# Optimization experiments

Measured on AMD Instinct MI355X. Metric: run time of the kernel, lower is better.

Reference implementation:

```python
import jax, jax.numpy as jnp
import numpy as np

IN_FEATURES = 128
OUT_FEATURES = 32
N_NODES = 2048
ALPHA = 0.2  # LeakyReLU negative slope
NEG_INF = -9e15


def setup_inputs() -> dict:
    key = jax.random.key(0)
    k1, k2, k3, k4 = jax.random.split(key, 4)
    h = jax.random.normal(k1, (N_NODES, IN_FEATURES), dtype=jnp.float32)
    adj = jax.random.randint(k2, (N_NODES, N_NODES), 0, 2, dtype=jnp.int32)
    # xavier_uniform-ish scaling for params
    W = jax.random.normal(k3, (2 * IN_FEATURES, OUT_FEATURES), dtype=jnp.float32) * 0.1
    a = jax.random.normal(k4, (OUT_FEATURES,), dtype=jnp.float32) * 0.2
    return {"h": h, "adj": adj, "W": W, "a": a}


def reference(h, adj, W, a):
    in_f = h.shape[1]
    Wh1 = h @ W[:in_f, :]   # [N, F]
    Wh2 = h @ W[in_f:, :]   # [N, F]
    # GATv2 score: e[i,k] = sum_f a[f] * leaky_relu(Wh1[i,f] + Wh2[k,f])
    e = jax.nn.leaky_relu(Wh1[:, None, :] + Wh2[None, :, :], negative_slope=ALPHA)  # [N, N, F]
    e = jnp.einsum('ikf,f->ik', e, a)  # [N, N]
    att = jnp.where(adj > 0, e, NEG_INF)
    att = jax.nn.softmax(att, axis=1)
    h_prime = att @ Wh1  # note: original aggregates Wh1, faithful to source
    return jax.nn.elu(h_prime)  # concat=True -> ELU
```

## Files before the change

### kernel.cpp

```cpp
#include <hip/hip_runtime.h>
#include <math.h>

#define N_NODES 2048
#define IN_F 128
#define OUT_F 32
#define NEG_INF -9e15f

__device__ __forceinline__ int swz(int k) { return k ^ (((k >> 7) & 7) << 2); }

__global__ __launch_bounds__(256) void precompute_wh(
    const float* __restrict__ h, const float* __restrict__ W,
    const float* __restrict__ a,
    float* __restrict__ Wh1, float* __restrict__ Wh2,
    float* __restrict__ Q, float* __restrict__ C)
{
    __shared__ float h_s[8][IN_F];
    const int t = threadIdx.x;
    const int i0 = blockIdx.x * 8;

    ((float4*)&h_s[0][0])[t] = ((const float4*)(h + (size_t)i0 * IN_F))[t];
    __syncthreads();

    const int f = t & 31;
    const int r = t >> 5;
    float acc1 = 0.f, acc2 = 0.f;
    #pragma unroll 8
    for (int c = 0; c < IN_F; ++c) {
        const float hv = h_s[r][c];
        acc1 = fmaf(hv, W[c * OUT_F + f], acc1);
        acc2 = fmaf(hv, W[(IN_F + c) * OUT_F + f], acc2);
    }
    Wh1[(i0 + r) * OUT_F + f] = acc1;
    Wh2[(i0 + r) * OUT_F + f] = acc2;

    float q = 0.6f * a[f] * acc2;
    #pragma unroll
    for (int off = 16; off > 0; off >>= 1) q += __shfl_xor(q, off, 64);
    if (f == 0) Q[i0 + r] = q;

    if (blockIdx.x == 0 && t < OUT_F) C[t] = 0.4f * a[t];
}

__global__ __launch_bounds__(256, 4) void gat_row(
    const float* __restrict__ Wh1, const float* __restrict__ Wh2,
    const float* __restrict__ Q, const float* __restrict__ C,
    const int* __restrict__ adj, float* __restrict__ out)
{
    __shared__ float p_s[2 * N_NODES];
    __shared__ float w1s[2][OUT_F];
    __shared__ float part[16][2][OUT_F];
    __shared__ float redA[4], redB[4], redC[4], redD[4];

    const int t = threadIdx.x;
    const int i0 = blockIdx.x * 2;

    if (t < 2 * OUT_F) w1s[t >> 5][t & 31] = Wh1[i0 * OUT_F + t];
    __syncthreads();

    const float4* w1f0 = (const float4*)&w1s[0][0];
    const float4* w1f1 = (const float4*)&w1s[1][0];

    float s00[4], s01[4], s10[4], s11[4];
    float m0 = NEG_INF, m1 = NEG_INF;

    #pragma unroll
    for (int kc = 0; kc < 4; ++kc) {
        const int k = 2 * t + 512 * kc;
        const float4* wr = (const float4*)(Wh2 + (size_t)k * OUT_F);
        float a00 = 0.f, a01 = 0.f, a10 = 0.f, a11 = 0.f;
        #pragma unroll
        for (int j = 0; j < 8; ++j) {
            const float4 w1a = w1f0[j];
            const float4 w1b = w1f1[j];
            const float4 qa = wr[j];
            const float4 qb = wr[8 + j];
            #pragma unroll
            for (int e = 0; e < 4; ++e) {
                const float cf  = C[4 * j + e];
                const float w2a = (e==0)?qa.x:(e==1)?qa.y:(e==2)?qa.z:qa.w;
                const float w2b = (e==0)?qb.x:(e==1)?qb.y:(e==2)?qb.z:qb.w;
                const float w10 = (e==0)?w1a.x:(e==1)?w1a.y:(e==2)?w1a.z:w1a.w;
                const float w11 = (e==0)?w1b.x:(e==1)?w1b.y:(e==2)?w1b.z:w1b.w;
                a00 = fmaf(cf, fabsf(w10 + w2a), a00);
                a01 = fmaf(cf, fabsf(w10 + w2b), a01);
                a10 = fmaf(cf, fabsf(w11 + w2a), a10);
                a11 = fmaf(cf, fabsf(w11 + w2b), a11);
            }
        }
        const int2 ad0   = *(const int2*)(adj + (size_t)(i0 + 0) * N_NODES + k);
        const int2 ad1   = *(const int2*)(adj + (size_t)(i0 + 1) * N_NODES + k);
        const float2 qk  = *(const float2*)(Q + k);
        const float v00 = (ad0.x > 0) ? a00 + qk.x : NEG_INF;
        const float v01 = (ad0.y > 0) ? a01 + qk.y : NEG_INF;
        const float v10 = (ad1.x > 0) ? a10 + qk.x : NEG_INF;
        const float v11 = (ad1.y > 0) ? a11 + qk.y : NEG_INF;
        s00[kc] = v00; s01[kc] = v01; s10[kc] = v10; s11[kc] = v11;
        m0 = fmaxf(m0, fmaxf(v00, v01));
        m1 = fmaxf(m1, fmaxf(v10, v11));
    }

    #pragma unroll
    for (int off = 32; off > 0; off >>= 1) {
        m0 = fmaxf(m0, __shfl_xor(m0, off, 64));
        m1 = fmaxf(m1, __shfl_xor(m1, off, 64));
    }
    const int lane = t & 63, wid = t >> 6;
    if (lane == 0) { redA[wid] = m0; redB[wid] = m1; }
    __syncthreads();
    const float M0 = fmaxf(fmaxf(redA[0], redA[1]), fmaxf(redA[2], redA[3]));
    const float M1 = fmaxf(fmaxf(redB[0], redB[1]), fmaxf(redB[2], redB[3]));

    float l0 = 0.f, l1 = 0.f;
    #pragma unroll
    for (int kc = 0; kc < 4; ++kc) {
        const int k = 2 * t + 512 * kc;
        const float p00 = __expf(s00[kc] - M0);
        const float p01 = __expf(s01[kc] - M0);
        const float p10 = __expf(s10[kc] - M1);
        const float p11 = __expf(s11[kc] - M1);
        *(float2*)&p_s[swz(k)]           = make_float2(p00, p01);
        *(float2*)&p_s[N_NODES + swz(k)] = make_float2(p10, p11);
        l0 += p00 + p01;
        l1 += p10 + p11;
    }
    #pragma unroll
    for (int off = 32; off > 0; off >>= 1) {
        l0 += __shfl_xor(l0, off, 64);
        l1 += __shfl_xor(l1, off, 64);
    }
    if (lane == 0) { redC[wid] = l0; redD[wid] = l1; }
    __syncthreads();
    const float L0 = redC[0] + redC[1] + redC[2] + redC[3];
    const float L1 = redD[0] + redD[1] + redD[2] + redD[3];

    const int f2 = t & 15;
    const int c  = t >> 4;
    float acc00 = 0.f, acc01 = 0.f, acc10 = 0.f, acc11 = 0.f;
    const int kb = c * 128;
    #pragma unroll 4
    for (int it = 0; it < 32; ++it) {
        const int k = kb + 4 * it;
        const float4 p0 = *(const float4*)&p_s[swz(k)];
        const float4 p1 = *(const float4*)&p_s[N_NODES + swz(k)];
        const float* wrow = Wh1 + (size_t)k * OUT_F + f2;
        const float wa0 = wrow[0],  wb0 = wrow[16];
        const float wa1 = wrow[32], wb1 = wrow[48];
        const float wa2 = wrow[64], wb2 = wrow[80];
        const float wa3 = wrow[96], wb3 = wrow[112];
        acc00 = fmaf(p0.x, wa0, acc00); acc01 = fmaf(p0.x, wb0, acc01);
        acc10 = fmaf(p1.x, wa0, acc10); acc11 = fmaf(p1.x, wb0, acc11);
        acc00 = fmaf(p0.y, wa1, acc00); acc01 = fmaf(p0.y, wb1, acc01);
        acc10 = fmaf(p1.y, wa1, acc10); acc11 = fmaf(p1.y, wb1, acc11);
        acc00 = fmaf(p0.z, wa2, acc00); acc01 = fmaf(p0.z, wb2, acc01);
        acc10 = fmaf(p1.z, wa2, acc10); acc11 = fmaf(p1.z, wb2, acc11);
        acc00 = fmaf(p0.w, wa3, acc00); acc01 = fmaf(p0.w, wb3, acc01);
        acc10 = fmaf(p1.w, wa3, acc10); acc11 = fmaf(p1.w, wb3, acc11);
    }
    part[c][0][f2]      = acc00;
    part[c][0][f2 + 16] = acc01;
    part[c][1][f2]      = acc10;
    part[c][1][f2 + 16] = acc11;
    __syncthreads();

    if (t < 2 * OUT_F) {
        const int ii = t >> 5, ff = t & 31;
        float s = 0.f;
        #pragma unroll
        for (int c2 = 0; c2 < 16; ++c2) s += part[c2][ii][ff];
        const float val = s / (ii == 0 ? L0 : L1);
        out[(i0 + ii) * OUT_F + ff] = (val > 0.f) ? val : (__expf(val) - 1.f);
    }
}

extern "C" void kernel_launch(void* const* d_in, const int* in_sizes, int n_in,
                              void* d_out, int out_size, void* d_ws, size_t ws_size,
                              hipStream_t stream) {
    const float* h   = (const float*)d_in[0];
    const int*   adj = (const int*)d_in[1];
    const float* W   = (const float*)d_in[2];
    const float* a   = (const float*)d_in[3];
    float* out = (float*)d_out;

    float* Wh1 = (float*)d_ws;
    float* Wh2 = Wh1 + N_NODES * OUT_F;
    float* Q   = Wh2 + N_NODES * OUT_F;
    float* C   = Q + N_NODES;

    precompute_wh<<<N_NODES / 8, 256, 0, stream>>>(h, W, a, Wh1, Wh2, Q, C);
    gat_row<<<N_NODES / 2, 256, 0, stream>>>(Wh1, Wh2, Q, C, adj, out);
}
```

Measured before the change: 125.2 us.

## Transpose Wh2 and process four rows per block for register reuse

The precompute kernel now writes Wh2 transposed (feature-major) through a shared-memory staging tile, so the score loop can load float4 runs of neighbour values per feature with coalesced access. The row kernel handles four query rows per block instead of two. Each thread computes 4x8 scores, which reuses each loaded Wh2 value across four rows and halves how often Wh2 and Wh1 are re-read during aggregation. The trade-off is higher register pressure: launch bounds drop to 2 blocks per SM, with fewer blocks in flight and fewer blocks overall.

```diff
diff --git a/kernel.cpp b/kernel.cpp
--- a/kernel.cpp
+++ b/kernel.cpp
@@ -11,10 +11,11 @@
 __global__ __launch_bounds__(256) void precompute_wh(
     const float* __restrict__ h, const float* __restrict__ W,
     const float* __restrict__ a,
-    float* __restrict__ Wh1, float* __restrict__ Wh2,
+    float* __restrict__ Wh1, float* __restrict__ Wh2T,
     float* __restrict__ Q, float* __restrict__ C)
 {
     __shared__ float h_s[8][IN_F];
+    __shared__ float tr[8][OUT_F];
     const int t = threadIdx.x;
     const int i0 = blockIdx.x * 8;
 
@@ -31,143 +32,175 @@
         acc2 = fmaf(hv, W[(IN_F + c) * OUT_F + f], acc2);
     }
     Wh1[(i0 + r) * OUT_F + f] = acc1;
-    Wh2[(i0 + r) * OUT_F + f] = acc2;
+    tr[r][f] = acc2;
 
     float q = 0.6f * a[f] * acc2;
     #pragma unroll
     for (int off = 16; off > 0; off >>= 1) q += __shfl_xor(q, off, 64);
     if (f == 0) Q[i0 + r] = q;
-
     if (blockIdx.x == 0 && t < OUT_F) C[t] = 0.4f * a[t];
+
+    __syncthreads();
+    const int f2 = t >> 3, r2 = t & 7;
+    Wh2T[f2 * N_NODES + i0 + r2] = tr[r2][f2];
 }
 
-__global__ __launch_bounds__(256, 4) void gat_row(
-    const float* __restrict__ Wh1, const float* __restrict__ Wh2,
+__global__ __launch_bounds__(256, 2) void gat_row(
+    const float* __restrict__ Wh1, const float* __restrict__ Wh2T,
     const float* __restrict__ Q, const float* __restrict__ C,
     const int* __restrict__ adj, float* __restrict__ out)
 {
-    __shared__ float p_s[2 * N_NODES];
-    __shared__ float w1s[2][OUT_F];
-    __shared__ float part[16][2][OUT_F];
-    __shared__ float redA[4], redB[4], redC[4], redD[4];
+    __shared__ float p_s[4][N_NODES];
+    __shared__ float w1s[4][OUT_F];
+    __shared__ float part[16][4][OUT_F];
+    __shared__ float redM[4][4], redL[4][4];
 
     const int t = threadIdx.x;
-    const int i0 = blockIdx.x * 2;
-
-    if (t < 2 * OUT_F) w1s[t >> 5][t & 31] = Wh1[i0 * OUT_F + t];
-    __syncthreads();
-
-    const float4* w1f0 = (const float4*)&w1s[0][0];
-    const float4* w1f1 = (const float4*)&w1s[1][0];
-
-    float s00[4], s01[4], s10[4], s11[4];
-    float m0 = NEG_INF, m1 = NEG_INF;
-
-    #pragma unroll
-    for (int kc = 0; kc < 4; ++kc) {
-        const int k = 2 * t + 512 * kc;
-        const float4* wr = (const float4*)(Wh2 + (size_t)k * OUT_F);
-        float a00 = 0.f, a01 = 0.f, a10 = 0.f, a11 = 0.f;
-        #pragma unroll
-        for (int j = 0; j < 8; ++j) {
-            const float4 w1a = w1f0[j];
-            const float4 w1b = w1f1[j];
-            const float4 qa = wr[j];
-            const float4 qb = wr[8 + j];
+    const int i0 = blockIdx.x * 4;
+
+    if (t < 4 * OUT_F) w1s[t >> 5][t & 31] = Wh1[i0 * OUT_F + t];
+    __syncthreads();
+
+    const int kA = 4 * t;
+    const int kB = N_NODES / 2 + 4 * t;
+
+    int4 adA[4], adB[4];
+    #pragma unroll
+    for (int i = 0; i < 4; ++i) {
+        adA[i] = *(const int4*)(adj + (size_t)(i0 + i) * N_NODES + kA);
+        adB[i] = *(const int4*)(adj + (size_t)(i0 + i) * N_NODES + kB);
+    }
+    const float4 QA = *(const float4*)(Q + kA);
+    const float4 QB = *(const float4*)(Q + kB);
+
+    float acc[4][8];
+    #pragma unroll
+    for (int i = 0; i < 4; ++i)
+        #pragma unroll
+        for (int s = 0; s < 8; ++s) acc[i][s] = 0.f;
+
+    #pragma unroll 2
+    for (int j = 0; j < 8; ++j) {
+        float4 w1v[4];
+        #pragma unroll
+        for (int i = 0; i < 4; ++i) w1v[i] = *(const float4*)&w1s[i][4 * j];
+        #pragma unroll
+        for (int e = 0; e < 4; ++e) {
+            const int f = 4 * j + e;
+            const float cf = C[f];
+            const float4 wA = *(const float4*)(Wh2T + (size_t)f * N_NODES + kA);
+            const float4 wB = *(const float4*)(Wh2T + (size_t)f * N_NODES + kB);
             #pragma unroll
-            for (int e = 0; e < 4; ++e) {
-                const float cf  = C[4 * j + e];
-                const float w2a = (e==0)?qa.x:(e==1)?qa.y:(e==2)?qa.z:qa.w;
-                const float w2b = (e==0)?qb.x:(e==1)?qb.y:(e==2)?qb.z:qb.w;
-                const float w10 = (e==0)?w1a.x:(e==1)?w1a.y:(e==2)?w1a.z:w1a.w;
-                const float w11 = (e==0)?w1b.x:(e==1)?w1b.y:(e==2)?w1b.z:w1b.w;
-                a00 = fmaf(cf, fabsf(w10 + w2a), a00);
-                a01 = fmaf(cf, fabsf(w10 + w2b), a01);
-                a10 = fmaf(cf, fabsf(w11 + w2a), a10);
-                a11 = fmaf(cf, fabsf(w11 + w2b), a11);
+            for (int i = 0; i < 4; ++i) {
+                const float w1 = (e==0)?w1v[i].x:(e==1)?w1v[i].y:(e==2)?w1v[i].z:w1v[i].w;
+                acc[i][0] = fmaf(cf, fabsf(w1 + wA.x), acc[i][0]);
+                acc[i][1] = fmaf(cf, fabsf(w1 + wA.y), acc[i][1]);
+                acc[i][2] = fmaf(cf, fabsf(w1 + wA.z), acc[i][2]);
+                acc[i][3] = fmaf(cf, fabsf(w1 + wA.w), acc[i][3]);
+                acc[i][4] = fmaf(cf, fabsf(w1 + wB.x), acc[i][4]);
+                acc[i][5] = fmaf(cf, fabsf(w1 + wB.y), acc[i][5]);
+                acc[i][6] = fmaf(cf, fabsf(w1 + wB.z), acc[i][6]);
+                acc[i][7] = fmaf(cf, fabsf(w1 + wB.w), acc[i][7]);
             }
         }
-        const int2 ad0   = *(const int2*)(adj + (size_t)(i0 + 0) * N_NODES + k);
-        const int2 ad1   = *(const int2*)(adj + (size_t)(i0 + 1) * N_NODES + k);
-        const float2 qk  = *(const float2*)(Q + k);
-        const float v00 = (ad0.x > 0) ? a00 + qk.x : NEG_INF;
-        const float v01 = (ad0.y > 0) ? a01 + qk.y : NEG_INF;
-        const float v10 = (ad1.x > 0) ? a10 + qk.x : NEG_INF;
-        const float v11 = (ad1.y > 0) ? a11 + qk.y : NEG_INF;
-        s00[kc] = v00; s01[kc] = v01; s10[kc] = v10; s11[kc] = v11;
-        m0 = fmaxf(m0, fmaxf(v00, v01));
-        m1 = fmaxf(m1, fmaxf(v10, v11));
-    }
-
-    #pragma unroll
-    for (int off = 32; off > 0; off >>= 1) {
-        m0 = fmaxf(m0, __shfl_xor(m0, off, 64));
-        m1 = fmaxf(m1, __shfl_xor(m1, off, 64));
+    }
+
+    float m[4];
+    #pragma unroll
+    for (int i = 0; i < 4; ++i) {
+        acc[i][0] = (adA[i].x > 0) ? acc[i][0] + QA.x : NEG_INF;
+        acc[i][1] = (adA[i].y > 0) ? acc[i][1] + QA.y : NEG_INF;
+        acc[i][2] = (adA[i].z > 0) ? acc[i][2] + QA.z : NEG_INF;
+        acc[i][3] = (adA[i].w > 0) ? acc[i][3] + QA.w : NEG_INF;
+        acc[i][4] = (adB[i].x > 0) ? acc[i][4] + QB.x : NEG_INF;
+        acc[i][5] = (adB[i].y > 0) ? acc[i][5] + QB.y : NEG_INF;
+        acc[i][6] = (adB[i].z > 0) ? acc[i][6] + QB.z : NEG_INF;
+        acc[i][7] = (adB[i].w > 0) ? acc[i][7] + QB.w : NEG_INF;
+        float mm = fmaxf(fmaxf(fmaxf(acc[i][0], acc[i][1]), fmaxf(acc[i][2], acc[i][3])),
+                         fmaxf(fmaxf(acc[i][4], acc[i][5]), fmaxf(acc[i][6], acc[i][7])));
+        #pragma unroll
+        for (int off = 32; off > 0; off >>= 1) mm = fmaxf(mm, __shfl_xor(mm, off, 64));
+        m[i] = mm;
     }
     const int lane = t & 63, wid = t >> 6;
-    if (lane == 0) { redA[wid] = m0; redB[wid] = m1; }
-    __syncthreads();
-    const float M0 = fmaxf(fmaxf(redA[0], redA[1]), fmaxf(redA[2], redA[3]));
-    const float M1 = fmaxf(fmaxf(redB[0], redB[1]), fmaxf(redB[2], redB[3]));
-
-    float l0 = 0.f, l1 = 0.f;
-    #pragma unroll
-    for (int kc = 0; kc < 4; ++kc) {
-        const int k = 2 * t + 512 * kc;
-        const float p00 = __expf(s00[kc] - M0);
-        const float p01 = __expf(s01[kc] - M0);
-        const float p10 = __expf(s10[kc] - M1);
-        const float p11 = __expf(s11[kc] - M1);
-        *(float2*)&p_s[swz(k)]           = make_float2(p00, p01);
-        *(float2*)&p_s[N_NODES + swz(k)] = make_float2(p10, p11);
-        l0 += p00 + p01;
-        l1 += p10 + p11;
-    }
-    #pragma unroll
-    for (int off = 32; off > 0; off >>= 1) {
-        l0 += __shfl_xor(l0, off, 64);
-        l1 += __shfl_xor(l1, off, 64);
-    }
-    if (lane == 0) { redC[wid] = l0; redD[wid] = l1; }
-    __syncthreads();
-    const float L0 = redC[0] + redC[1] + redC[2] + redC[3];
-    const float L1 = redD[0] + redD[1] + redD[2] + redD[3];
+    if (lane == 0) {
+        redM[0][wid] = m[0]; redM[1][wid] = m[1];
+        redM[2][wid] = m[2]; redM[3][wid] = m[3];
+    }
+    __syncthreads();
+
+    float L[4];
+    #pragma unroll
+    for (int i = 0; i < 4; ++i) {
+        const float M = fmaxf(fmaxf(redM[i][0], redM[i][1]), fmaxf(redM[i][2], redM[i][3]));
+        const float p0 = __expf(acc[i][0] - M);
+        const float p1 = __expf(acc[i][1] - M);
+        const float p2 = __expf(acc[i][2] - M);
+        const float p3 = __expf(acc[i][3] - M);
+        const float p4 = __expf(acc[i][4] - M);
+        const float p5 = __expf(acc[i][5] - M);
+        const float p6 = __expf(acc[i][6] - M);
+        const float p7 = __expf(acc[i][7] - M);
+        *(float4*)&p_s[i][swz(kA)] = make_float4(p0, p1, p2, p3);
+        *(float4*)&p_s[i][swz(kB)] = make_float4(p4, p5, p6, p7);
+        float ll = (p0 + p1) + (p2 + p3) + ((p4 + p5) + (p6 + p7));
+        #pragma unroll
+        for (int off = 32; off > 0; off >>= 1) ll += __shfl_xor(ll, off, 64);
+        L[i] = ll;
+    }
+    if (lane == 0) {
+        redL[0][wid] = L[0]; redL[1][wid] = L[1];
+        redL[2][wid] = L[2]; redL[3][wid] = L[3];
+    }
+    __syncthreads();
 
     const int f2 = t & 15;
     const int c  = t >> 4;
-    float acc00 = 0.f, acc01 = 0.f, acc10 = 0.f, acc11 = 0.f;
+    float a00=0.f, a01=0.f, a10=0.f, a11=0.f, a20=0.f, a21=0.f, a30=0.f, a31=0.f;
     const int kb = c * 128;
     #pragma unroll 4
     for (int it = 0; it < 32; ++it) {
         const int k = kb + 4 * it;
-        const float4 p0 = *(const float4*)&p_s[swz(k)];
-        const float4 p1 = *(const float4*)&p_s[N_NODES + swz(k)];
+        const int ks = swz(k);
+        const float4 p0 = *(const float4*)&p_s[0][ks];
+        const float4 p1 = *(const float4*)&p_s[1][ks];
+        const float4 p2 = *(const float4*)&p_s[2][ks];
+        const float4 p3 = *(const float4*)&p_s[3][ks];
         const float* wrow = Wh1 + (size_t)k * OUT_F + f2;
         const float wa0 = wrow[0],  wb0 = wrow[16];
         const float wa1 = wrow[32], wb1 = wrow[48];
         const float wa2 = wrow[64], wb2 = wrow[80];
         const float wa3 = wrow[96], wb3 = wrow[112];
-        acc00 = fmaf(p0.x, wa0, acc00); acc01 = fmaf(p0.x, wb0, acc01);
-        acc10 = fmaf(p1.x, wa0, acc10); acc11 = fmaf(p1.x, wb0, acc11);
-        acc00 = fmaf(p0.y, wa1, acc00); acc01 = fmaf(p0.y, wb1, acc01);
-        acc10 = fmaf(p1.y, wa1, acc10); acc11 = fmaf(p1.y, wb1, acc11);
-        acc00 = fmaf(p0.z, wa2, acc00); acc01 = fmaf(p0.z, wb2, acc01);
-        acc10 = fmaf(p1.z, wa2, acc10); acc11 = fmaf(p1.z, wb2, acc11);
-        acc00 = fmaf(p0.w, wa3, acc00); acc01 = fmaf(p0.w, wb3, acc01);
-        acc10 = fmaf(p1.w, wa3, acc10); acc11 = fmaf(p1.w, wb3, acc11);
-    }
-    part[c][0][f2]      = acc00;
-    part[c][0][f2 + 16] = acc01;
-    part[c][1][f2]      = acc10;
-    part[c][1][f2 + 16] = acc11;
-    __syncthreads();
-
-    if (t < 2 * OUT_F) {
+        a00 = fmaf(p0.x, wa0, a00); a01 = fmaf(p0.x, wb0, a01);
+        a10 = fmaf(p1.x, wa0, a10); a11 = fmaf(p1.x, wb0, a11);
+        a20 = fmaf(p2.x, wa0, a20); a21 = fmaf(p2.x, wb0, a21);
+        a30 = fmaf(p3.x, wa0, a30); a31 = fmaf(p3.x, wb0, a31);
+        a00 = fmaf(p0.y, wa1, a00); a01 = fmaf(p0.y, wb1, a01);
+        a10 = fmaf(p1.y, wa1, a10); a11 = fmaf(p1.y, wb1, a11);
+        a20 = fmaf(p2.y, wa1, a20); a21 = fmaf(p2.y, wb1, a21);
+        a30 = fmaf(p3.y, wa1, a30); a31 = fmaf(p3.y, wb1, a31);
+        a00 = fmaf(p0.z, wa2, a00); a01 = fmaf(p0.z, wb2, a01);
+        a10 = fmaf(p1.z, wa2, a10); a11 = fmaf(p1.z, wb2, a11);
+        a20 = fmaf(p2.z, wa2, a20); a21 = fmaf(p2.z, wb2, a21);
+        a30 = fmaf(p3.z, wa2, a30); a31 = fmaf(p3.z, wb2, a31);
+        a00 = fmaf(p0.w, wa3, a00); a01 = fmaf(p0.w, wb3, a01);
+        a10 = fmaf(p1.w, wa3, a10); a11 = fmaf(p1.w, wb3, a11);
+        a20 = fmaf(p2.w, wa3, a20); a21 = fmaf(p2.w, wb3, a21);
+        a30 = fmaf(p3.w, wa3, a30); a31 = fmaf(p3.w, wb3, a31);
+    }
+    part[c][0][f2] = a00; part[c][0][f2 + 16] = a01;
+    part[c][1][f2] = a10; part[c][1][f2 + 16] = a11;
+    part[c][2][f2] = a20; part[c][2][f2 + 16] = a21;
+    part[c][3][f2] = a30; part[c][3][f2 + 16] = a31;
+    __syncthreads();
+
+    if (t < 4 * OUT_F) {
         const int ii = t >> 5, ff = t & 31;
         float s = 0.f;
         #pragma unroll
         for (int c2 = 0; c2 < 16; ++c2) s += part[c2][ii][ff];
-        const float val = s / (ii == 0 ? L0 : L1);
+        const float Lf = redL[ii][0] + redL[ii][1] + redL[ii][2] + redL[ii][3];
+        const float val = s / Lf;
         out[(i0 + ii) * OUT_F + ff] = (val > 0.f) ? val : (__expf(val) - 1.f);
     }
 }
@@ -181,11 +214,11 @@
     const float* a   = (const float*)d_in[3];
     float* out = (float*)d_out;
 
-    float* Wh1 = (float*)d_ws;
-    float* Wh2 = Wh1 + N_NODES * OUT_F;
-    float* Q   = Wh2 + N_NODES * OUT_F;
-    float* C   = Q + N_NODES;
-
-    precompute_wh<<<N_NODES / 8, 256, 0, stream>>>(h, W, a, Wh1, Wh2, Q, C);
-    gat_row<<<N_NODES / 2, 256, 0, stream>>>(Wh1, Wh2, Q, C, adj, out);
+    float* Wh1  = (float*)d_ws;
+    float* Wh2T = Wh1 + N_NODES * OUT_F;
+    float* Q    = Wh2T + N_NODES * OUT_F;
+    float* C    = Q + N_NODES;
+
+    precompute_wh<<<N_NODES / 8, 256, 0, stream>>>(h, W, a, Wh1, Wh2T, Q, C);
+    gat_row<<<N_NODES / 4, 256, 0, stream>>>(Wh1, Wh2T, Q, C, adj, out);
 }
```

After: 102.5 us. -18.1%, faster.
